# Kernel optimization log

Measured on AMD Instinct MI355X. Metric: run time of the kernel, lower is better.

Reference implementation:

```python
import jax, jax.numpy as jnp
import numpy as np

HIDDEN = 160
LAYERS = 32
CLASSES = 10
IN_DIM = 784


def setup_inputs() -> dict:
    key = jax.random.key(0)
    ks = jax.random.split(key, 6)
    B = 65536
    x = jax.random.normal(ks[0], (B, IN_DIM), dtype=jnp.float32)
    # embed: torch nn.Linear(IN_DIM, HIDDEN); store weight as [IN_DIM, HIDDEN] so y = x @ W + b
    embed_w = jax.random.normal(ks[1], (IN_DIM, HIDDEN), dtype=jnp.float32) / np.sqrt(IN_DIM)
    embed_b = jnp.zeros((HIDDEN,), dtype=jnp.float32)
    # 32 residual-layer weights, kaiming_normal (fan_in=HIDDEN, relu gain sqrt(2)) scaled by 0.1
    layer_w = jax.random.normal(ks[2], (LAYERS, HIDDEN, HIDDEN), dtype=jnp.float32) * (np.sqrt(2.0 / HIDDEN) * 0.1)
    head_w = jax.random.normal(ks[3], (HIDDEN, CLASSES), dtype=jnp.float32) / np.sqrt(HIDDEN)
    head_b = jnp.zeros((CLASSES,), dtype=jnp.float32)
    return {"x": x, "embed_w": embed_w, "embed_b": embed_b,
            "layer_w": layer_w, "head_w": head_w, "head_b": head_b}


def reference(x, embed_w, embed_b, layer_w, head_w, head_b):
    # x: [B, 784] (already flat)
    h = x @ embed_w + embed_b  # [B, H]

    def step(h, W):
        # y = relu(h @ W) + h
        return jax.nn.relu(h @ W) + h, None

    h, _ = jax.lax.scan(step, h, layer_w)  # scan over the 32 layer weights
    return h @ head_w + head_b  # [B, CLASSES]
```

## Files before the change

kernel.cpp:

```cpp
#include <hip/hip_runtime.h>
#include <cstdint>
#include <cstddef>


typedef __attribute__((ext_vector_type(8))) short bfrag8;
typedef __attribute__((ext_vector_type(16))) float f32x16;
typedef __attribute__((ext_vector_type(4))) uint32_t u32x4;

#define MFMA32(a, b, c) __builtin_amdgcn_mfma_f32_32x32x16_bf16((a), (b), (c), 0, 0, 0)

#define NFRAG_TOTAL 1855

static __device__ __forceinline__ uint16_t f2bf16u(float v) {
    uint32_t u = __builtin_bit_cast(uint32_t, v);
    uint32_t r = u + 0x7FFFu + ((u >> 16) & 1u);
    return (uint16_t)(r >> 16);
}
static __device__ __forceinline__ uint32_t pack2_bf16(float lo, float hi) {
    return (uint32_t)f2bf16u(lo) | ((uint32_t)f2bf16u(hi) << 16);
}
static __device__ __forceinline__ uint32_t cvtpk(float lo, float hi) {
    uint32_t r;
    asm("v_cvt_pk_bf16_f32 %0, %1, %2" : "=v"(r) : "v"(lo), "v"(hi));
    return r;
}
static __device__ __forceinline__ void gl_lds16(const void* g, void* l) {
    __builtin_amdgcn_global_load_lds(
        (const __attribute__((address_space(1))) uint32_t*)g,
        (__attribute__((address_space(3))) uint32_t*)l, 16, 0, 0);
}

__global__ __launch_bounds__(256) void resmlp_prep(
    const float* __restrict__ embed_w, const float* __restrict__ layer_w,
    const float* __restrict__ head_w, uint16_t* __restrict__ ws)
{
    const int fb = blockIdx.x * 4 + (threadIdx.x >> 6);
    if (fb >= NFRAG_TOTAL) return;
    const int l = threadIdx.x & 63;
    const int h = l >> 5, m32 = l & 31;
    float v[8];
    if (fb < 245) {
        const int kt = fb / 5, mt = fb % 5;
        const int m = mt * 32 + m32;
        const int kb = kt * 16 + h * 8;
#pragma unroll
        for (int j = 0; j < 8; ++j)
            v[j] = embed_w[(size_t)(kb + j) * 160 + m];
    } else if (fb < 1845) {
        const int t = fb - 245, L = t / 50, r = t % 50, kt = r / 5, mt = r % 5;
        const int m = mt * 32 + m32;
        const float* W = layer_w + (size_t)L * 25600;
        const int kb = 32 * (kt >> 1) + 16 * (kt & 1) + 4 * h;
#pragma unroll
        for (int j = 0; j < 8; ++j)
            v[j] = W[(size_t)(kb + (j & 3) + 8 * (j >> 2)) * 160 + m];
    } else {
        const int kt = fb - 1845;
        const int kb = 32 * (kt >> 1) + 16 * (kt & 1) + 4 * h;
#pragma unroll
        for (int j = 0; j < 8; ++j)
            v[j] = (m32 < 10) ? head_w[(kb + (j & 3) + 8 * (j >> 2)) * 10 + m32] : 0.f;
    }
    u32x4 wv;
    wv.x = pack2_bf16(v[0], v[1]);
    wv.y = pack2_bf16(v[2], v[3]);
    wv.z = pack2_bf16(v[4], v[5]);
    wv.w = pack2_bf16(v[6], v[7]);
    *(u32x4*)((char*)ws + (size_t)fb * 1024 + l * 16) = wv;
}

struct StageP { int S, C, D; };
static __device__ __forceinline__ StageP stage_params(int u, int hf) {
    StageP p;
    if (u < 5)       { p.S = u * 50 + hf * 25;            p.C = (u == 4 && hf) ? 20 : 25; p.D = hf * 25600; }
    else if (u < 37) { p.S = 245 + (u - 5) * 50 + hf * 25; p.C = 25;                      p.D = hf * 25600; }
    else             { p.S = 1845 + hf * 5;                p.C = 5;                        p.D = hf * 5120;  }
    return p;
}

template<int K0, int K1>
static __device__ __forceinline__ void embed_loadx(const float* __restrict__ xb,
                                                   float4 (&xv)[10])
{
#pragma unroll
    for (int kt = K0; kt < K1; ++kt) {
        xv[2 * (kt - K0)]     = *(const float4*)(xb + kt * 16);
        xv[2 * (kt - K0) + 1] = *(const float4*)(xb + kt * 16 + 4);
    }
}

template<int K0, int K1>
static __device__ __forceinline__ void embed_mfma(const float4 (&xv)[10],
    const uint16_t* __restrict__ lds, f32x16 (&acc)[5], int lane8)
{
#pragma unroll
    for (int kt = K0; kt < K1; ++kt) {
        const float4 v0 = xv[2 * (kt - K0)], v1 = xv[2 * (kt - K0) + 1];
        u32x4 bw;
        bw.x = cvtpk(v0.x, v0.y);
        bw.y = cvtpk(v0.z, v0.w);
        bw.z = cvtpk(v1.x, v1.y);
        bw.w = cvtpk(v1.z, v1.w);
        const bfrag8 b = __builtin_bit_cast(bfrag8, bw);
#pragma unroll
        for (int mt = 0; mt < 5; ++mt) {
            const bfrag8 a = *(const bfrag8*)(lds + (kt * 5 + mt) * 512 + lane8);
            acc[mt] = MFMA32(a, b, acc[mt]);
        }
    }
}

template<int K0, int K1, int NMT>
static __device__ __forceinline__ void layer_mfma(
    const uint16_t* __restrict__ lds, f32x16 (&acc)[5],
    const f32x16 (&resid)[5], int lane8)
{
#pragma unroll
    for (int kt = K0; kt < K1; ++kt) {
        const int ms = kt >> 1, rb = (kt & 1) * 8;
        u32x4 bw;
        bw.x = cvtpk(resid[ms][rb + 0], resid[ms][rb + 1]);
        bw.y = cvtpk(resid[ms][rb + 2], resid[ms][rb + 3]);
        bw.z = cvtpk(resid[ms][rb + 4], resid[ms][rb + 5]);
        bw.w = cvtpk(resid[ms][rb + 6], resid[ms][rb + 7]);
        const bfrag8 b = __builtin_bit_cast(bfrag8, bw);
#pragma unroll
        for (int mt = 0; mt < NMT; ++mt) {
            const bfrag8 a = *(const bfrag8*)(lds + (kt * NMT + mt) * 512 + lane8);
            acc[mt] = MFMA32(a, b, acc[mt]);
        }
    }
}

__global__ __launch_bounds__(256, 2) void resmlp_main(
    const float* __restrict__ x,
    const float* __restrict__ embed_b,
    const float* __restrict__ head_b,
    const uint16_t* __restrict__ ws,
    float* __restrict__ out)
{
    extern __shared__ __align__(16) uint16_t lds[];
    const int tid  = threadIdx.x;
    const int wave = tid >> 6, lane = tid & 63;
    const int hi = lane >> 5, ln = lane & 31;
    const int lane8 = lane * 8;
    const int batch = blockIdx.x * 128 + wave * 32 + ln;

    f32x16 acc[5], resid[5];
#pragma unroll
    for (int mt = 0; mt < 5; ++mt)
#pragma unroll
        for (int r = 0; r < 16; ++r) acc[mt][r] = 0.f;

    auto do_stage = [&](int u, int hf) {
        const StageP p = stage_params(u, hf);
        const char* src = (const char*)ws + (size_t)p.S * 1024 + lane * 16;
        char* dst = (char*)lds + p.D + lane * 16;
        for (int i = wave; i < p.C; i += 4)
            gl_lds16(src + (size_t)i * 1024, dst + i * 1024);
    };

    do_stage(0, 0);
    __syncthreads();

    for (int c = 0; c < 5; ++c) {
        const float* xb = x + (size_t)batch * 784 + c * 160 + hi * 8;
        float4 xv[10];
        embed_loadx<0, 5>(xb, xv);
        do_stage(c, 1);
        embed_mfma<0, 5>(xv, lds, acc, lane8);
        __syncthreads();
        if (c < 4) {
            embed_loadx<5, 10>(xb, xv);
            do_stage(c + 1, 0);
            embed_mfma<5, 10>(xv, lds, acc, lane8);
        } else {
            embed_loadx<5, 9>(xb, xv);
            do_stage(5, 0);
            embed_mfma<5, 9>(xv, lds, acc, lane8);
        }
        __syncthreads();
    }

    for (int L = 0; L < 32; ++L) {
        do_stage(5 + L, 1);
        if (L == 0) {
#pragma unroll
            for (int mt = 0; mt < 5; ++mt)
#pragma unroll
                for (int q2 = 0; q2 < 4; ++q2) {
                    const float4 b4 = *(const float4*)(embed_b + mt * 32 + q2 * 8 + hi * 4);
                    resid[mt][q2 * 4 + 0] = acc[mt][q2 * 4 + 0] + b4.x;
                    resid[mt][q2 * 4 + 1] = acc[mt][q2 * 4 + 1] + b4.y;
                    resid[mt][q2 * 4 + 2] = acc[mt][q2 * 4 + 2] + b4.z;
                    resid[mt][q2 * 4 + 3] = acc[mt][q2 * 4 + 3] + b4.w;
                }
        } else {
#pragma unroll
            for (int mt = 0; mt < 5; ++mt)
#pragma unroll
                for (int r = 0; r < 16; ++r)
                    resid[mt][r] += fmaxf(acc[mt][r], 0.f);
        }
#pragma unroll
        for (int mt = 0; mt < 5; ++mt)
#pragma unroll
            for (int r = 0; r < 16; ++r) acc[mt][r] = 0.f;

        layer_mfma<0, 5, 5>(lds, acc, resid, lane8);
        __syncthreads();
        do_stage(L < 31 ? 6 + L : 37, 0);
        layer_mfma<5, 10, 5>(lds, acc, resid, lane8);
        __syncthreads();
    }

    do_stage(37, 1);
#pragma unroll
    for (int mt = 0; mt < 5; ++mt)
#pragma unroll
        for (int r = 0; r < 16; ++r)
            resid[mt][r] += fmaxf(acc[mt][r], 0.f);
#pragma unroll
    for (int r = 0; r < 16; ++r) acc[0][r] = 0.f;

    layer_mfma<0, 5, 1>(lds, acc, resid, lane8);
    __syncthreads();
    layer_mfma<5, 10, 1>(lds, acc, resid, lane8);

    float* op = out + (size_t)batch * 10;
    if (hi == 0) {
        op[0] = acc[0][0] + head_b[0];
        op[1] = acc[0][1] + head_b[1];
        op[2] = acc[0][2] + head_b[2];
        op[3] = acc[0][3] + head_b[3];
        op[8] = acc[0][4] + head_b[8];
        op[9] = acc[0][5] + head_b[9];
    } else {
        op[4] = acc[0][0] + head_b[4];
        op[5] = acc[0][1] + head_b[5];
        op[6] = acc[0][2] + head_b[6];
        op[7] = acc[0][3] + head_b[7];
    }
}

extern "C" void kernel_launch(void* const* d_in, const int* in_sizes, int n_in,
                              void* d_out, int out_size, void* d_ws, size_t ws_size,
                              hipStream_t stream) {
    (void)in_sizes; (void)n_in; (void)out_size; (void)ws_size;
    const float* x       = (const float*)d_in[0];
    const float* embed_w = (const float*)d_in[1];
    const float* embed_b = (const float*)d_in[2];
    const float* layer_w = (const float*)d_in[3];
    const float* head_w  = (const float*)d_in[4];
    const float* head_b  = (const float*)d_in[5];
    float* out = (float*)d_out;

    uint16_t* ws = (uint16_t*)d_ws;

    const int dynLds = 51200;
    (void)hipFuncSetAttribute((const void*)resmlp_main,
                              hipFuncAttributeMaxDynamicSharedMemorySize, dynLds);

    resmlp_prep<<<(NFRAG_TOTAL + 3) / 4, 256, 0, stream>>>(embed_w, layer_w, head_w, ws);
    resmlp_main<<<512, 256, dynLds, stream>>>(x, embed_b, head_b, ws, out);
}
```

Before: 397.3 us.

## Triple-buffer weight staging in LDS with vmcnt waits instead of syncthreads

```diff
diff --git a/kernel.cpp b/kernel.cpp
--- a/kernel.cpp
+++ b/kernel.cpp
@@ -10,6 +10,10 @@
 #define MFMA32(a, b, c) __builtin_amdgcn_mfma_f32_32x32x16_bf16((a), (b), (c), 0, 0, 0)
 
 #define NFRAG_TOTAL 1855
+#define HALF_BYTES  25600
+#define HALF_ELEMS  12800
+
+#define WAITVM(N) asm volatile("s_waitcnt vmcnt(" #N ")" ::: "memory")
 
 static __device__ __forceinline__ uint16_t f2bf16u(float v) {
     uint32_t u = __builtin_bit_cast(uint32_t, v);
@@ -69,33 +73,26 @@
     *(u32x4*)((char*)ws + (size_t)fb * 1024 + l * 16) = wv;
 }
 
-struct StageP { int S, C, D; };
-static __device__ __forceinline__ StageP stage_params(int u, int hf) {
-    StageP p;
-    if (u < 5)       { p.S = u * 50 + hf * 25;            p.C = (u == 4 && hf) ? 20 : 25; p.D = hf * 25600; }
-    else if (u < 37) { p.S = 245 + (u - 5) * 50 + hf * 25; p.C = 25;                      p.D = hf * 25600; }
-    else             { p.S = 1845 + hf * 5;                p.C = 5;                        p.D = hf * 5120;  }
-    return p;
-}
-
-template<int K0, int K1>
+template<int NK>
 static __device__ __forceinline__ void embed_loadx(const float* __restrict__ xb,
                                                    float4 (&xv)[10])
 {
 #pragma unroll
-    for (int kt = K0; kt < K1; ++kt) {
-        xv[2 * (kt - K0)]     = *(const float4*)(xb + kt * 16);
-        xv[2 * (kt - K0) + 1] = *(const float4*)(xb + kt * 16 + 4);
-    }
-}
-
-template<int K0, int K1>
-static __device__ __forceinline__ void embed_mfma(const float4 (&xv)[10],
-    const uint16_t* __restrict__ lds, f32x16 (&acc)[5], int lane8)
-{
-#pragma unroll
-    for (int kt = K0; kt < K1; ++kt) {
-        const float4 v0 = xv[2 * (kt - K0)], v1 = xv[2 * (kt - K0) + 1];
+    for (int kt = 0; kt < NK; ++kt) {
+        xv[2 * kt]     = *(const float4*)(xb + kt * 16);
+        xv[2 * kt + 1] = *(const float4*)(xb + kt * 16 + 4);
+    }
+}
+
+template<int NK>
+static __device__ __forceinline__ void embed_mfma_h(
+    const uint16_t* __restrict__ buf, const float4 (&xv)[10],
+    f32x16 (&acc)[5], int lane8)
+{
+    __builtin_amdgcn_s_setprio(1);
+#pragma unroll
+    for (int kt = 0; kt < NK; ++kt) {
+        const float4 v0 = xv[2 * kt], v1 = xv[2 * kt + 1];
         u32x4 bw;
         bw.x = cvtpk(v0.x, v0.y);
         bw.y = cvtpk(v0.z, v0.w);
@@ -104,20 +101,22 @@
         const bfrag8 b = __builtin_bit_cast(bfrag8, bw);
 #pragma unroll
         for (int mt = 0; mt < 5; ++mt) {
-            const bfrag8 a = *(const bfrag8*)(lds + (kt * 5 + mt) * 512 + lane8);
+            const bfrag8 a = *(const bfrag8*)(buf + (kt * 5 + mt) * 512 + lane8);
             acc[mt] = MFMA32(a, b, acc[mt]);
         }
     }
-}
-
-template<int K0, int K1, int NMT>
-static __device__ __forceinline__ void layer_mfma(
-    const uint16_t* __restrict__ lds, f32x16 (&acc)[5],
+    __builtin_amdgcn_s_setprio(0);
+}
+
+template<int KT0, int NMT, bool ZC>
+static __device__ __forceinline__ void layer_mfma_h(
+    const uint16_t* __restrict__ buf, f32x16 (&acc)[5],
     const f32x16 (&resid)[5], int lane8)
 {
-#pragma unroll
-    for (int kt = K0; kt < K1; ++kt) {
-        const int ms = kt >> 1, rb = (kt & 1) * 8;
+    __builtin_amdgcn_s_setprio(1);
+#pragma unroll
+    for (int i = 0; i < 5; ++i) {
+        const int kt = KT0 + i, ms = kt >> 1, rb = (kt & 1) * 8;
         u32x4 bw;
         bw.x = cvtpk(resid[ms][rb + 0], resid[ms][rb + 1]);
         bw.y = cvtpk(resid[ms][rb + 2], resid[ms][rb + 3]);
@@ -126,10 +125,18 @@
         const bfrag8 b = __builtin_bit_cast(bfrag8, bw);
 #pragma unroll
         for (int mt = 0; mt < NMT; ++mt) {
-            const bfrag8 a = *(const bfrag8*)(lds + (kt * NMT + mt) * 512 + lane8);
-            acc[mt] = MFMA32(a, b, acc[mt]);
+            const bfrag8 a = *(const bfrag8*)(buf + (i * NMT + mt) * 512 + lane8);
+            if (ZC && i == 0) {
+                f32x16 z;
+#pragma unroll
+                for (int r = 0; r < 16; ++r) z[r] = 0.f;
+                acc[mt] = MFMA32(a, b, z);
+            } else {
+                acc[mt] = MFMA32(a, b, acc[mt]);
+            }
         }
     }
+    __builtin_amdgcn_s_setprio(0);
 }
 
 __global__ __launch_bounds__(256, 2) void resmlp_main(
@@ -142,9 +149,9 @@
     extern __shared__ __align__(16) uint16_t lds[];
     const int tid  = threadIdx.x;
     const int wave = tid >> 6, lane = tid & 63;
-    const int hi = lane >> 5, ln = lane & 31;
+    const int hi = lane >> 5;
     const int lane8 = lane * 8;
-    const int batch = blockIdx.x * 128 + wave * 32 + ln;
+    const int batch = blockIdx.x * 128 + wave * 32 + (lane & 31);
 
     f32x16 acc[5], resid[5];
 #pragma unroll
@@ -152,38 +159,43 @@
 #pragma unroll
         for (int r = 0; r < 16; ++r) acc[mt][r] = 0.f;
 
-    auto do_stage = [&](int u, int hf) {
-        const StageP p = stage_params(u, hf);
-        const char* src = (const char*)ws + (size_t)p.S * 1024 + lane * 16;
-        char* dst = (char*)lds + p.D + lane * 16;
-        for (int i = wave; i < p.C; i += 4)
+    auto do_stage = [&](int u) {
+        int S, C;
+        if (u < 10)      { S = (u >> 1) * 50 + (u & 1) * 25; C = (u == 9) ? 20 : 25; }
+        else if (u < 74) { S = 245 + (u - 10) * 25;          C = 25; }
+        else             { S = 1845 + (u - 74) * 5;          C = 5; }
+        const char* src = (const char*)ws + (size_t)S * 1024 + lane * 16;
+        char* dst = (char*)lds + (u % 3) * HALF_BYTES + lane * 16;
+        for (int i = wave; i < C; i += 4)
             gl_lds16(src + (size_t)i * 1024, dst + i * 1024);
     };
 
-    do_stage(0, 0);
-    __syncthreads();
+    do_stage(0);
+    do_stage(1);
+
+    const float* xrow = x + (size_t)batch * 784 + hi * 8;
 
     for (int c = 0; c < 5; ++c) {
-        const float* xb = x + (size_t)batch * 784 + c * 160 + hi * 8;
         float4 xv[10];
-        embed_loadx<0, 5>(xb, xv);
-        do_stage(c, 1);
-        embed_mfma<0, 5>(xv, lds, acc, lane8);
-        __syncthreads();
-        if (c < 4) {
-            embed_loadx<5, 10>(xb, xv);
-            do_stage(c + 1, 0);
-            embed_mfma<5, 10>(xv, lds, acc, lane8);
-        } else {
-            embed_loadx<5, 9>(xb, xv);
-            do_stage(5, 0);
-            embed_mfma<5, 9>(xv, lds, acc, lane8);
-        }
-        __syncthreads();
-    }
-
-    for (int L = 0; L < 32; ++L) {
-        do_stage(5 + L, 1);
+        __builtin_amdgcn_s_barrier();
+        embed_loadx<5>(xrow + c * 160, xv);
+        do_stage(2 * c + 2);
+        WAITVM(11);
+        embed_mfma_h<5>(lds + ((2 * c) % 3) * HALF_ELEMS, xv, acc, lane8);
+        __builtin_amdgcn_s_barrier();
+        if (c < 4) embed_loadx<5>(xrow + c * 160 + 80, xv);
+        else       embed_loadx<4>(xrow + c * 160 + 80, xv);
+        do_stage(2 * c + 3);
+        WAITVM(11);
+        if (c < 4) embed_mfma_h<5>(lds + ((2 * c + 1) % 3) * HALF_ELEMS, xv, acc, lane8);
+        else       embed_mfma_h<4>(lds + ((2 * c + 1) % 3) * HALF_ELEMS, xv, acc, lane8);
+    }
+
+    for (int L = 0; L < 31; ++L) {
+        const int u = 10 + 2 * L;
+        const int bA = u % 3, bB = (u + 1) % 3;
+        __builtin_amdgcn_s_barrier();
+        do_stage(u + 2);
         if (L == 0) {
 #pragma unroll
             for (int mt = 0; mt < 5; ++mt)
@@ -202,30 +214,43 @@
                 for (int r = 0; r < 16; ++r)
                     resid[mt][r] += fmaxf(acc[mt][r], 0.f);
         }
+        WAITVM(12);
+        layer_mfma_h<0, 5, true>(lds + bA * HALF_ELEMS, acc, resid, lane8);
+        __builtin_amdgcn_s_barrier();
+        do_stage(u + 3);
+        WAITVM(12);
+        layer_mfma_h<5, 5, false>(lds + bB * HALF_ELEMS, acc, resid, lane8);
+    }
+
+    {
+        __builtin_amdgcn_s_barrier();
+        do_stage(74);
 #pragma unroll
         for (int mt = 0; mt < 5; ++mt)
 #pragma unroll
-            for (int r = 0; r < 16; ++r) acc[mt][r] = 0.f;
-
-        layer_mfma<0, 5, 5>(lds, acc, resid, lane8);
-        __syncthreads();
-        do_stage(L < 31 ? 6 + L : 37, 0);
-        layer_mfma<5, 10, 5>(lds, acc, resid, lane8);
-        __syncthreads();
-    }
-
-    do_stage(37, 1);
-#pragma unroll
-    for (int mt = 0; mt < 5; ++mt)
-#pragma unroll
-        for (int r = 0; r < 16; ++r)
-            resid[mt][r] += fmaxf(acc[mt][r], 0.f);
-#pragma unroll
-    for (int r = 0; r < 16; ++r) acc[0][r] = 0.f;
-
-    layer_mfma<0, 5, 1>(lds, acc, resid, lane8);
-    __syncthreads();
-    layer_mfma<5, 10, 1>(lds, acc, resid, lane8);
+            for (int r = 0; r < 16; ++r)
+                resid[mt][r] += fmaxf(acc[mt][r], 0.f);
+        WAITVM(7);
+        layer_mfma_h<0, 5, true>(lds + 0 * HALF_ELEMS, acc, resid, lane8);
+        __builtin_amdgcn_s_barrier();
+        do_stage(75);
+        WAITVM(2);
+        layer_mfma_h<5, 5, false>(lds + 1 * HALF_ELEMS, acc, resid, lane8);
+    }
+
+    {
+        __builtin_amdgcn_s_barrier();
+#pragma unroll
+        for (int mt = 0; mt < 5; ++mt)
+#pragma unroll
+            for (int r = 0; r < 16; ++r)
+                resid[mt][r] += fmaxf(acc[mt][r], 0.f);
+        WAITVM(1);
+        layer_mfma_h<0, 1, true>(lds + 2 * HALF_ELEMS, acc, resid, lane8);
+        __builtin_amdgcn_s_barrier();
+        WAITVM(0);
+        layer_mfma_h<5, 1, false>(lds + 0 * HALF_ELEMS, acc, resid, lane8);
+    }
 
     float* op = out + (size_t)batch * 10;
     if (hi == 0) {
@@ -257,7 +282,7 @@
 
     uint16_t* ws = (uint16_t*)d_ws;
 
-    const int dynLds = 51200;
+    const int dynLds = 3 * HALF_BYTES;
     (void)hipFuncSetAttribute((const void*)resmlp_main,
                               hipFuncAttributeMaxDynamicSharedMemorySize, dynLds);
 
```

New measurement: 398.8 us. Within noise of the previous version (+0.4%).
